# Performance work log

Measured on AMD Instinct MI355X. Metric: run time of the kernel, lower is better.

Reference implementation:

```python
import jax, jax.numpy as jnp
import numpy as np

D_K = 64
N_HEADS = 16
D_MODEL = 1024


def setup_inputs() -> dict:
    key = jax.random.key(0)
    ks = jax.random.split(key, 12)
    N, T = 2, 2048
    H = D_K * N_HEADS
    s = 1.0 / np.sqrt(D_MODEL)
    inp = {
        "q": jax.random.normal(ks[0], (N, T, D_MODEL), jnp.float32),
        "k": jax.random.normal(ks[1], (N, T, D_MODEL), jnp.float32),
        "v": jax.random.normal(ks[2], (N, T, D_MODEL), jnp.float32),
        "mask": jax.random.randint(ks[3], (N, T), 0, 2, jnp.int32),
        "Wq": jax.random.normal(ks[4], (D_MODEL, H), jnp.float32) * s,
        "bq": jax.random.normal(ks[5], (H,), jnp.float32) * 0.02,
        "Wk": jax.random.normal(ks[6], (D_MODEL, H), jnp.float32) * s,
        "bk": jax.random.normal(ks[7], (H,), jnp.float32) * 0.02,
        "Wv": jax.random.normal(ks[8], (D_MODEL, H), jnp.float32) * s,
        "bv": jax.random.normal(ks[9], (H,), jnp.float32) * 0.02,
        "Wo": jax.random.normal(ks[10], (H, D_MODEL), jnp.float32) * (1.0 / np.sqrt(H)),
        "bo": jax.random.normal(ks[11], (D_MODEL,), jnp.float32) * 0.02,
    }
    return inp


def reference(q, k, v, mask, Wq, bq, Wk, bk, Wv, bv, Wo, bo):
    N, T, _ = q.shape
    # project and split heads: [N, T, H*dk] -> [N, nH, T, dk]
    def split(x):
        return x.reshape(N, T, N_HEADS, D_K).transpose(0, 2, 1, 3)
    qh = split(q @ Wq + bq)
    kh = split(k @ Wk + bk)
    vh = split(v @ Wv + bv)
    scores = jnp.einsum("bhqd,bhkd->bhqk", qh, kh) / np.sqrt(D_K)
    # key padding mask: mask[:, None, None, :] == 0 -> -inf
    scores = jnp.where(mask[:, None, None, :] == 0, -jnp.inf, scores)
    attn = jax.nn.softmax(scores, axis=-1)
    A = jnp.einsum("bhqk,bhkd->bhqd", attn, vh)
    A = A.transpose(0, 2, 1, 3).reshape(N, T, N_HEADS * D_K)
    return A @ Wo + bo
```

## Files before the change

### kernel.cpp

```cpp
#include <hip/hip_runtime.h>

#define T_SEQ 2048
#define DM 1024
#define NH 16
#define DKH 64
#define NB 2
#define M_ROWS (NB * T_SEQ)
#define QSCALE 0.18033688011112042f

using bf16x8 = __attribute__((ext_vector_type(8))) __bf16;
using f32x4  = __attribute__((ext_vector_type(4))) float;
using halfx4 = __attribute__((ext_vector_type(4))) __fp16;
using halfx8 = __attribute__((ext_vector_type(8))) __fp16;
using halfx2 = __attribute__((ext_vector_type(2))) __fp16;
using uintx4 = __attribute__((ext_vector_type(4))) unsigned;

__device__ __forceinline__ short f2bf(float f) {
  unsigned u = __builtin_bit_cast(unsigned, f);
  u += 0x7fffu + ((u >> 16) & 1u);
  return (short)(u >> 16);
}

#if defined(__has_builtin) && __has_builtin(__builtin_amdgcn_cvt_pk_bf16_f32)
using bf16x2 = __attribute__((ext_vector_type(2))) __bf16;
__device__ __forceinline__ short2 pk2(float a, float b) {
  bf16x2 r = __builtin_amdgcn_cvt_pk_bf16_f32(a, b);
  return __builtin_bit_cast(short2, r);
}
#else
__device__ __forceinline__ short2 pk2(float a, float b) {
  short2 r; r.x = f2bf(a); r.y = f2bf(b); return r;
}
#endif

__device__ __forceinline__ short2 pkh(float a, float b) {
  halfx2 r = __builtin_amdgcn_cvt_pkrtz(a, b);
  return __builtin_bit_cast(short2, r);
}

#if defined(__has_builtin) && __has_builtin(__builtin_amdgcn_exp2f)
__device__ __forceinline__ float fexp2(float x) { return __builtin_amdgcn_exp2f(x); }
#else
__device__ __forceinline__ float fexp2(float x) { return exp2f(x); }
#endif

#if defined(__has_builtin) && __has_builtin(__builtin_amdgcn_permlane32_swap) && \
    __has_builtin(__builtin_amdgcn_permlane16_swap)
using uintx2 = __attribute__((ext_vector_type(2))) unsigned;
__device__ __forceinline__ void swap32(unsigned& a, unsigned& b) {
  uintx2 r = __builtin_amdgcn_permlane32_swap(a, b, false, false);
  a = r.x; b = r.y;
}
__device__ __forceinline__ void swap16(unsigned& a, unsigned& b) {
  uintx2 r = __builtin_amdgcn_permlane16_swap(a, b, false, false);
  a = r.x; b = r.y;
}
#else
__device__ __forceinline__ void swap32(unsigned& a, unsigned& b) {
  asm volatile("v_permlane32_swap_b32 %0, %1" : "+v"(a), "+v"(b));
}
__device__ __forceinline__ void swap16(unsigned& a, unsigned& b) {
  asm volatile("v_permlane16_swap_b32 %0, %1" : "+v"(a), "+v"(b));
}
#endif

#define GLD16(g, l)                                                            \
  __builtin_amdgcn_global_load_lds(                                            \
      (const __attribute__((address_space(1))) void*)(g),                      \
      (__attribute__((address_space(3))) void*)(l), 16, 0, 0)

__global__ __launch_bounds__(256) void prep_x(
    const float* __restrict__ q, const float* __restrict__ k,
    const float* __restrict__ v, const int* __restrict__ mask,
    short* __restrict__ dst, float* __restrict__ mf) {
  const float* s = blockIdx.z == 0 ? q : (blockIdx.z == 1 ? k : v);
  short* d = dst + (size_t)blockIdx.z * (M_ROWS * DM);
  const int n4 = M_ROWS * DM / 4;
  for (int i = blockIdx.x * 256 + threadIdx.x; i < n4; i += gridDim.x * 256) {
    float4 f = *(const float4*)(s + i * 4);
    short2 a = pk2(f.x, f.y), b = pk2(f.z, f.w);
    short4 o = {a.x, a.y, b.x, b.y};
    *(short4*)(d + i * 4) = o;
  }
  if (blockIdx.z == 0 && blockIdx.x < 4) {
    int i = (blockIdx.x * 256 + threadIdx.x) * 4;
    int4 m = *(const int4*)(mask + i);
    float4 o = {m.x ? 0.f : -1e38f, m.y ? 0.f : -1e38f,
                m.z ? 0.f : -1e38f, m.w ? 0.f : -1e38f};
    *(float4*)(mf + i) = o;
  }
}

__global__ __launch_bounds__(256) void prep_w(
    const float* __restrict__ w0, const float* __restrict__ w1,
    const float* __restrict__ w2, const float* __restrict__ w3,
    short* __restrict__ dst) {
  __shared__ short T[64][72];
  const float* W = blockIdx.z == 0 ? w0 : blockIdx.z == 1 ? w1
                   : blockIdx.z == 2 ? w2 : w3;
  short* D = dst + (size_t)blockIdx.z * (DM * DM);
  const int k0 = blockIdx.x * 64, n0 = blockIdx.y * 64;
  const int r = threadIdx.x >> 2, cs = (threadIdx.x & 3) * 16;
#pragma unroll
  for (int j = 0; j < 4; ++j) {
    float4 f = *(const float4*)(W + (size_t)(k0 + r) * DM + n0 + cs + j * 4);
    short2 a = pk2(f.x, f.y), b = pk2(f.z, f.w);
    short4 o = {a.x, a.y, b.x, b.y};
    *(short4*)&T[r][cs + j * 4] = o;
  }
  __syncthreads();
  short tmp[16];
#pragma unroll
  for (int i = 0; i < 16; ++i) tmp[i] = T[cs + i][r];
  *(int4*)(D + (size_t)(n0 + r) * DM + k0 + cs) = *(const int4*)&tmp[0];
  *(int4*)(D + (size_t)(n0 + r) * DM + k0 + cs + 8) = *(const int4*)&tmp[8];
}

__global__ __launch_bounds__(512) void gemm_qkv(
    const short* __restrict__ A_, const short* __restrict__ Bt_,
    const float* __restrict__ b0, const float* __restrict__ b1,
    const float* __restrict__ b2, short* __restrict__ Y) {
  __shared__ short As[2][4096];
  __shared__ short Bs[2][4096];
  const int z = blockIdx.z;
  const short* A = A_ + (size_t)z * (M_ROWS * DM);
  const short* Bt = Bt_ + (size_t)z * (DM * DM);
  short* Yz = Y + (size_t)z * ((size_t)M_ROWS * DM);
  const float* bias = z == 0 ? b0 : (z == 1 ? b1 : b2);
  const int m0 = blockIdx.x * 128, n0 = blockIdx.y * 128;
  const int tid = threadIdx.x, w = tid >> 6, lane = tid & 63;
  const int quad = lane >> 4, lm = lane & 15, wa = w & 1, wb = w >> 1;

  const short* Ag = A + (size_t)(m0 + w * 16 + lm) * DM + quad * 8;
  const short* Bg = Bt + (size_t)(n0 + w * 16 + lm) * DM + quad * 8;

  f32x4 acc[4][2];
#pragma unroll
  for (int i = 0; i < 4; ++i)
#pragma unroll
    for (int j = 0; j < 2; ++j) acc[i][j] = (f32x4){0.f, 0.f, 0.f, 0.f};

  GLD16(Ag, &As[0][w * 512]);
  GLD16(Bg, &Bs[0][w * 512]);

  for (int kt = 0; kt < DM / 32; ++kt) {
    const int cb = kt & 1;
    __syncthreads();
    if (kt + 1 < DM / 32) {
      GLD16(Ag + (kt + 1) * 32, &As[cb ^ 1][w * 512]);
      GLD16(Bg + (kt + 1) * 32, &Bs[cb ^ 1][w * 512]);
    }
    bf16x8 af[4], bfr[2];
#pragma unroll
    for (int i = 0; i < 4; ++i)
      af[i] = *(const bf16x8*)&As[cb][(wa * 4 + i) * 512 + quad * 128 + lm * 8];
#pragma unroll
    for (int j = 0; j < 2; ++j)
      bfr[j] = *(const bf16x8*)&Bs[cb][(wb * 2 + j) * 512 + quad * 128 + lm * 8];
#pragma unroll
    for (int mi = 0; mi < 4; ++mi)
#pragma unroll
      for (int j = 0; j < 2; ++j)
        acc[mi][j] = __builtin_amdgcn_mfma_f32_16x16x32_bf16(
            af[mi], bfr[j], acc[mi][j], 0, 0, 0);
  }

  if (z < 2) {
#pragma unroll
    for (int j = 0; j < 2; ++j) {
      const int f = n0 + (wb * 2 + j) * 16 + lm;
      const float bv = bias[f];
      const int h = f >> 6, dk = f & 63;
#pragma unroll
      for (int mi = 0; mi < 4; ++mi)
#pragma unroll
        for (int r = 0; r < 4; ++r) {
          const int m = m0 + (wa * 4 + mi) * 16 + quad * 4 + r;
          float val = acc[mi][j][r] + bv;
          if (z == 0) val *= QSCALE;
          const int b = m >> 11, tt = m & (T_SEQ - 1);
          Yz[(((size_t)(b * NH + h) << 11) + tt) * DKH + dk] = f2bf(val);
        }
    }
  } else {
#pragma unroll
    for (int j = 0; j < 2; ++j) {
      const int f = n0 + (wb * 2 + j) * 16 + lm;
      const float bv = bias[f];
      const int h = f >> 6, dk = f & 63;
#pragma unroll
      for (int mi = 0; mi < 4; ++mi) {
        const int t = m0 + (wa * 4 + mi) * 16 + quad * 4;
        const int b = t >> 11, tt = t & (T_SEQ - 1);
        short2 a = pkh(acc[mi][j][0] + bv, acc[mi][j][1] + bv);
        short2 c = pkh(acc[mi][j][2] + bv, acc[mi][j][3] + bv);
        short4 o = {a.x, a.y, c.x, c.y};
        *(short4*)(Yz + (((size_t)(b * NH + h) * DKH + dk) << 11) + tt) = o;
      }
    }
  }
}

__global__ __launch_bounds__(512) void gemm_out(
    const short* __restrict__ A, const short* __restrict__ Bt,
    const float* __restrict__ bias, float* __restrict__ Yf) {
  __shared__ short As[2][4096];
  __shared__ short Bs[2][4096];
  const int m0 = blockIdx.x * 128, n0 = blockIdx.y * 128;
  const int tid = threadIdx.x, w = tid >> 6, lane = tid & 63;
  const int quad = lane >> 4, lm = lane & 15, wa = w & 1, wb = w >> 1;

  const short* Ag = A + (size_t)(m0 + w * 16 + lm) * DM + quad * 8;
  const short* Bg = Bt + (size_t)(n0 + w * 16 + lm) * DM + quad * 8;

  f32x4 acc[4][2];
#pragma unroll
  for (int i = 0; i < 4; ++i)
#pragma unroll
    for (int j = 0; j < 2; ++j) acc[i][j] = (f32x4){0.f, 0.f, 0.f, 0.f};

  GLD16(Ag, &As[0][w * 512]);
  GLD16(Bg, &Bs[0][w * 512]);

  for (int kt = 0; kt < DM / 32; ++kt) {
    const int cb = kt & 1;
    __syncthreads();
    if (kt + 1 < DM / 32) {
      GLD16(Ag + (kt + 1) * 32, &As[cb ^ 1][w * 512]);
      GLD16(Bg + (kt + 1) * 32, &Bs[cb ^ 1][w * 512]);
    }
    bf16x8 af[4], bfr[2];
#pragma unroll
    for (int i = 0; i < 4; ++i)
      af[i] = *(const bf16x8*)&As[cb][(wa * 4 + i) * 512 + quad * 128 + lm * 8];
#pragma unroll
    for (int j = 0; j < 2; ++j)
      bfr[j] = *(const bf16x8*)&Bs[cb][(wb * 2 + j) * 512 + quad * 128 + lm * 8];
#pragma unroll
    for (int mi = 0; mi < 4; ++mi)
#pragma unroll
      for (int j = 0; j < 2; ++j)
        acc[mi][j] = __builtin_amdgcn_mfma_f32_16x16x32_bf16(
            af[mi], bfr[j], acc[mi][j], 0, 0, 0);
  }

#pragma unroll
  for (int j = 0; j < 2; ++j) {
    const int n = n0 + (wb * 2 + j) * 16 + lm;
    const float bv = bias[n];
#pragma unroll
    for (int mi = 0; mi < 4; ++mi)
#pragma unroll
      for (int r = 0; r < 4; ++r) {
        const int m = m0 + (wa * 4 + mi) * 16 + quad * 4 + r;
        Yf[(size_t)m * DM + n] = acc[mi][j][r] + bv;
      }
  }
}

__global__ __launch_bounds__(512) void attn_kernel(
    const short* __restrict__ Qh, const short* __restrict__ Kh,
    const short* __restrict__ Vt, const float* __restrict__ mf,
    short* __restrict__ Ao) {
  __shared__ short Ks[4][8192];
  __shared__ short Vs[4][8192];
  __shared__ float Ms[T_SEQ];
  const int id = blockIdx.x + gridDim.x * blockIdx.y;
  const int bh = id & 31, qt = id >> 5;
  const int b = bh >> 4, h = bh & (NH - 1);
  const int tid = threadIdx.x, w = tid >> 6, lane = tid & 63;
  const int quad = lane >> 4, lm = lane & 15;
  const size_t base = (size_t)bh * T_SEQ * DKH;
  const float* mp = mf + b * T_SEQ;
  const int q0 = qt * 256 + w * 32;

  const short* qpA = Qh + base + (size_t)(q0 + lm) * DKH;
  const short* qpB = qpA + (size_t)16 * DKH;
  const bf16x8 qbA0 = *(const bf16x8*)(qpA + quad * 8);
  const bf16x8 qbA1 = *(const bf16x8*)(qpA + 32 + quad * 8);
  const bf16x8 qbB0 = *(const bf16x8*)(qpB + quad * 8);
  const bf16x8 qbB1 = *(const bf16x8*)(qpB + 32 + quad * 8);

  const int sw = w & 3;
  const bool isV = w >= 4;
  const short* Kg = Kh + base + (size_t)(sw * 16 + lm) * DKH + quad * 8;
  const short* Vg = Vt + base + (size_t)(sw * 16 + lm) * T_SEQ + quad * 8;

  GLD16(mp + w * 256 + lane * 4, &Ms[w * 256]);

  f32x4 otA[4], otB[4];
#pragma unroll
  for (int i = 0; i < 4; ++i) {
    otA[i] = (f32x4){0.f, 0.f, 0.f, 0.f};
    otB[i] = (f32x4){0.f, 0.f, 0.f, 0.f};
  }
  float lA = 0.f, lB = 0.f;

  auto stageK = [&](int buf, int key) {
    GLD16(Kg + (size_t)key * DKH, &Ks[buf][sw * 1024]);
    GLD16(Kg + (size_t)key * DKH + 32, &Ks[buf][sw * 1024 + 512]);
    GLD16(Kg + (size_t)(key + 64) * DKH, &Ks[buf][(sw + 4) * 1024]);
    GLD16(Kg + (size_t)(key + 64) * DKH + 32, &Ks[buf][(sw + 4) * 1024 + 512]);
  };
  auto stageV = [&](int buf, int key) {
    GLD16(Vg + key, &Vs[buf][sw * 2048]);
    GLD16(Vg + key + 32, &Vs[buf][sw * 2048 + 512]);
    GLD16(Vg + key + 64, &Vs[buf][sw * 2048 + 1024]);
    GLD16(Vg + key + 96, &Vs[buf][sw * 2048 + 1536]);
  };

  if (!isV) { stageK(0, 0); stageK(1, 128); }
  else      { stageV(0, 0); stageV(1, 128); }

  for (int kt = 0; kt < T_SEQ / 128; ++kt) {
    const int cb = kt & 3;
    const int key0 = kt * 128;
    if (kt + 2 < T_SEQ / 128) {
      if (!isV) stageK((kt + 2) & 3, key0 + 256);
      else      stageV((kt + 2) & 3, key0 + 256);
    }
    if (kt + 2 < T_SEQ / 128)      asm volatile("s_waitcnt vmcnt(8)" ::: "memory");
    else if (kt + 1 < T_SEQ / 128) asm volatile("s_waitcnt vmcnt(4)" ::: "memory");
    else                           asm volatile("s_waitcnt vmcnt(0)" ::: "memory");
    __builtin_amdgcn_s_barrier();
    __builtin_amdgcn_sched_barrier(0);

    halfx8 pbA[4], pbB[4];
#pragma unroll
    for (int kp = 0; kp < 4; ++kp) {
      unsigned peA0, peA1, poA0, poA1;
      unsigned peB0, peB1, poB0, poB1;
#pragma unroll
      for (int hf = 0; hf < 2; ++hf) {
        const int nt = kp * 2 + hf;
        bf16x8 ka0 = *(const bf16x8*)&Ks[cb][nt * 1024 + quad * 128 + lm * 8];
        bf16x8 ka1 = *(const bf16x8*)&Ks[cb][nt * 1024 + 512 + quad * 128 + lm * 8];
        f32x4 sA = (f32x4){0.f, 0.f, 0.f, 0.f};
        sA = __builtin_amdgcn_mfma_f32_16x16x32_bf16(ka0, qbA0, sA, 0, 0, 0);
        sA = __builtin_amdgcn_mfma_f32_16x16x32_bf16(ka1, qbA1, sA, 0, 0, 0);
        f32x4 sB = (f32x4){0.f, 0.f, 0.f, 0.f};
        sB = __builtin_amdgcn_mfma_f32_16x16x32_bf16(ka0, qbB0, sB, 0, 0, 0);
        sB = __builtin_amdgcn_mfma_f32_16x16x32_bf16(ka1, qbB1, sB, 0, 0, 0);
        const float4 m4 = *(const float4*)&Ms[key0 + nt * 16 + quad * 4];
        float a0 = fexp2(sA[0] + m4.x);
        float a1 = fexp2(sA[1] + m4.y);
        float a2 = fexp2(sA[2] + m4.z);
        float a3 = fexp2(sA[3] + m4.w);
        lA += (a0 + a1) + (a2 + a3);
        float b0 = fexp2(sB[0] + m4.x);
        float b1 = fexp2(sB[1] + m4.y);
        float b2 = fexp2(sB[2] + m4.z);
        float b3 = fexp2(sB[3] + m4.w);
        lB += (b0 + b1) + (b2 + b3);
        unsigned loA = __builtin_bit_cast(unsigned, pkh(a0, a1));
        unsigned hiA = __builtin_bit_cast(unsigned, pkh(a2, a3));
        unsigned loB = __builtin_bit_cast(unsigned, pkh(b0, b1));
        unsigned hiB = __builtin_bit_cast(unsigned, pkh(b2, b3));
        if (hf == 0) {
          peA0 = loA; peA1 = hiA; peB0 = loB; peB1 = hiB;
        } else {
          poA0 = loA; poA1 = hiA; poB0 = loB; poB1 = hiB;
        }
      }
      {
        unsigned x0 = peA0, y0 = poA0, x1 = peA1, y1 = poA1;
        swap32(x0, y0); swap16(x0, y0);
        swap32(x1, y1); swap16(x1, y1);
        pbA[kp] = __builtin_bit_cast(halfx8, (uintx4){x0, x1, y0, y1});
      }
      {
        unsigned x0 = peB0, y0 = poB0, x1 = peB1, y1 = poB1;
        swap32(x0, y0); swap16(x0, y0);
        swap32(x1, y1); swap16(x1, y1);
        pbB[kp] = __builtin_bit_cast(halfx8, (uintx4){x0, x1, y0, y1});
      }
    }

#pragma unroll
    for (int nt2 = 0; nt2 < 4; ++nt2) {
#pragma unroll
      for (int kp = 0; kp < 4; ++kp) {
        halfx8 va =
            *(const halfx8*)&Vs[cb][nt2 * 2048 + kp * 512 + quad * 128 + lm * 8];
        otA[nt2] =
            __builtin_amdgcn_mfma_f32_16x16x32_f16(va, pbA[kp], otA[nt2], 0, 0, 0);
        otB[nt2] =
            __builtin_amdgcn_mfma_f32_16x16x32_f16(va, pbB[kp], otB[nt2], 0, 0, 0);
      }
    }
  }
  lA += __shfl_xor(lA, 16, 64);
  lA += __shfl_xor(lA, 32, 64);
  lB += __shfl_xor(lB, 16, 64);
  lB += __shfl_xor(lB, 32, 64);
  const float invA = 1.f / lA;
  const float invB = 1.f / lB;
  const size_t rowA = (size_t)(b * T_SEQ + q0 + lm) * DM + h * DKH;
  const size_t rowB = rowA + (size_t)16 * DM;
#pragma unroll
  for (int nt = 0; nt < 4; ++nt) {
    short2 a = pk2(otA[nt][0] * invA, otA[nt][1] * invA);
    short2 c = pk2(otA[nt][2] * invA, otA[nt][3] * invA);
    short4 o4 = {a.x, a.y, c.x, c.y};
    *(short4*)(Ao + rowA + nt * 16 + quad * 4) = o4;
    short2 e = pk2(otB[nt][0] * invB, otB[nt][1] * invB);
    short2 g = pk2(otB[nt][2] * invB, otB[nt][3] * invB);
    short4 o5 = {e.x, e.y, g.x, g.y};
    *(short4*)(Ao + rowB + nt * 16 + quad * 4) = o5;
  }
}

extern "C" void kernel_launch(void* const* d_in, const int* in_sizes, int n_in,
                              void* d_out, int out_size, void* d_ws, size_t ws_size,
                              hipStream_t stream) {
  const float* q = (const float*)d_in[0];
  const float* k = (const float*)d_in[1];
  const float* v = (const float*)d_in[2];
  const int* mk = (const int*)d_in[3];
  const float* Wq = (const float*)d_in[4];
  const float* bq = (const float*)d_in[5];
  const float* Wk = (const float*)d_in[6];
  const float* bk = (const float*)d_in[7];
  const float* Wv = (const float*)d_in[8];
  const float* bv = (const float*)d_in[9];
  const float* Wo = (const float*)d_in[10];
  const float* bo = (const float*)d_in[11];

  const size_t XE = (size_t)M_ROWS * DM;
  const size_t WE = (size_t)DM * DM;
  short* xb = (short*)d_ws;
  short* Wt = xb + 3 * XE;
  short* Qh = Wt + 4 * WE;
  float* mf = (float*)(Qh + 3 * XE);
  short* Ao = xb;

  prep_x<<<dim3(1024, 1, 3), 256, 0, stream>>>(q, k, v, mk, xb, mf);
  prep_w<<<dim3(16, 16, 4), 256, 0, stream>>>(Wq, Wk, Wv, Wo, Wt);
  gemm_qkv<<<dim3(M_ROWS / 128, DM / 128, 3), 512, 0, stream>>>(
      xb, Wt, bq, bk, bv, Qh);
  attn_kernel<<<dim3(T_SEQ / 256, NB * NH), 512, 0, stream>>>(
      Qh, Qh + XE, Qh + 2 * XE, mf, Ao);
  gemm_out<<<dim3(M_ROWS / 128, DM / 128), 512, 0, stream>>>(
      Ao, Wt + 3 * WE, bo, (float*)d_out);
}
```

Measured before the change: 246.2 us.

## Deepen GEMM global-to-LDS pipeline to prefetch distance two with four buffers

```diff
diff --git a/kernel.cpp b/kernel.cpp
--- a/kernel.cpp
+++ b/kernel.cpp
@@ -120,8 +120,8 @@
     const short* __restrict__ A_, const short* __restrict__ Bt_,
     const float* __restrict__ b0, const float* __restrict__ b1,
     const float* __restrict__ b2, short* __restrict__ Y) {
-  __shared__ short As[2][4096];
-  __shared__ short Bs[2][4096];
+  __shared__ short As[4][4096];
+  __shared__ short Bs[4][4096];
   const int z = blockIdx.z;
   const short* A = A_ + (size_t)z * (M_ROWS * DM);
   const short* Bt = Bt_ + (size_t)z * (DM * DM);
@@ -130,6 +130,7 @@
   const int m0 = blockIdx.x * 128, n0 = blockIdx.y * 128;
   const int tid = threadIdx.x, w = tid >> 6, lane = tid & 63;
   const int quad = lane >> 4, lm = lane & 15, wa = w & 1, wb = w >> 1;
+  const int NT = DM / 32;
 
   const short* Ag = A + (size_t)(m0 + w * 16 + lm) * DM + quad * 8;
   const short* Bg = Bt + (size_t)(n0 + w * 16 + lm) * DM + quad * 8;
@@ -142,14 +143,21 @@
 
   GLD16(Ag, &As[0][w * 512]);
   GLD16(Bg, &Bs[0][w * 512]);
-
-  for (int kt = 0; kt < DM / 32; ++kt) {
-    const int cb = kt & 1;
-    __syncthreads();
-    if (kt + 1 < DM / 32) {
-      GLD16(Ag + (kt + 1) * 32, &As[cb ^ 1][w * 512]);
-      GLD16(Bg + (kt + 1) * 32, &Bs[cb ^ 1][w * 512]);
-    }
+  GLD16(Ag + 32, &As[1][w * 512]);
+  GLD16(Bg + 32, &Bs[1][w * 512]);
+
+  for (int kt = 0; kt < NT; ++kt) {
+    const int cb = kt & 3;
+    if (kt + 2 < NT) {
+      GLD16(Ag + (kt + 2) * 32, &As[(kt + 2) & 3][w * 512]);
+      GLD16(Bg + (kt + 2) * 32, &Bs[(kt + 2) & 3][w * 512]);
+    }
+    if (kt + 2 < NT)      asm volatile("s_waitcnt vmcnt(4)" ::: "memory");
+    else if (kt + 1 < NT) asm volatile("s_waitcnt vmcnt(2)" ::: "memory");
+    else                  asm volatile("s_waitcnt vmcnt(0)" ::: "memory");
+    __builtin_amdgcn_s_barrier();
+    __builtin_amdgcn_sched_barrier(0);
+
     bf16x8 af[4], bfr[2];
 #pragma unroll
     for (int i = 0; i < 4; ++i)
@@ -204,11 +212,12 @@
 __global__ __launch_bounds__(512) void gemm_out(
     const short* __restrict__ A, const short* __restrict__ Bt,
     const float* __restrict__ bias, float* __restrict__ Yf) {
-  __shared__ short As[2][4096];
-  __shared__ short Bs[2][4096];
+  __shared__ short As[4][4096];
+  __shared__ short Bs[4][4096];
   const int m0 = blockIdx.x * 128, n0 = blockIdx.y * 128;
   const int tid = threadIdx.x, w = tid >> 6, lane = tid & 63;
   const int quad = lane >> 4, lm = lane & 15, wa = w & 1, wb = w >> 1;
+  const int NT = DM / 32;
 
   const short* Ag = A + (size_t)(m0 + w * 16 + lm) * DM + quad * 8;
   const short* Bg = Bt + (size_t)(n0 + w * 16 + lm) * DM + quad * 8;
@@ -221,14 +230,21 @@
 
   GLD16(Ag, &As[0][w * 512]);
   GLD16(Bg, &Bs[0][w * 512]);
-
-  for (int kt = 0; kt < DM / 32; ++kt) {
-    const int cb = kt & 1;
-    __syncthreads();
-    if (kt + 1 < DM / 32) {
-      GLD16(Ag + (kt + 1) * 32, &As[cb ^ 1][w * 512]);
-      GLD16(Bg + (kt + 1) * 32, &Bs[cb ^ 1][w * 512]);
-    }
+  GLD16(Ag + 32, &As[1][w * 512]);
+  GLD16(Bg + 32, &Bs[1][w * 512]);
+
+  for (int kt = 0; kt < NT; ++kt) {
+    const int cb = kt & 3;
+    if (kt + 2 < NT) {
+      GLD16(Ag + (kt + 2) * 32, &As[(kt + 2) & 3][w * 512]);
+      GLD16(Bg + (kt + 2) * 32, &Bs[(kt + 2) & 3][w * 512]);
+    }
+    if (kt + 2 < NT)      asm volatile("s_waitcnt vmcnt(4)" ::: "memory");
+    else if (kt + 1 < NT) asm volatile("s_waitcnt vmcnt(2)" ::: "memory");
+    else                  asm volatile("s_waitcnt vmcnt(0)" ::: "memory");
+    __builtin_amdgcn_s_barrier();
+    __builtin_amdgcn_sched_barrier(0);
+
     bf16x8 af[4], bfr[2];
 #pragma unroll
     for (int i = 0; i < 4; ++i)
```

New measurement: 240.4 us. 1.02x faster.
